# Kernel tuning notes

Hardware: AMD Instinct MI355X
Metric: run time of the kernel (lower is better)

The kernel has to match this reference:

```python
import jax, jax.numpy as jnp
import numpy as np

B, N, CH, DIM, SLOTS, ITERS, HID = 32, 4096, 256, 256, 11, 3, 512
EPS_ATTN = 1e-8
LN_EPS = 1e-3


def _ln(x, g, b):
    m = jnp.mean(x, axis=-1, keepdims=True)
    v = jnp.mean((x - m) ** 2, axis=-1, keepdims=True)
    return (x - m) * jax.lax.rsqrt(v + LN_EPS) * g + b


def setup_inputs() -> dict:
    key = jax.random.key(0)
    ks = jax.random.split(key, 16)
    s = lambda d: 1.0 / np.sqrt(d)
    return {
        "inputs": jax.random.normal(ks[0], (B, N, CH), jnp.float32),
        "noise": jax.random.normal(ks[1], (B, SLOTS, DIM), jnp.float32),
        "slots_mu": jax.random.uniform(ks[2], (1, 1, DIM), jnp.float32, -0.15, 0.15),
        "slots_log_sigma": jax.random.uniform(ks[3], (1, 1, DIM), jnp.float32, -0.15, 0.15),
        "Wq": jax.random.normal(ks[4], (DIM, DIM), jnp.float32) * s(DIM),
        "Wk": jax.random.normal(ks[5], (DIM, CH), jnp.float32) * s(CH),
        "Wv": jax.random.normal(ks[6], (DIM, CH), jnp.float32) * s(CH),
        "W_ih": jax.random.normal(ks[7], (3 * DIM, DIM), jnp.float32) * s(DIM),
        "W_hh": jax.random.normal(ks[8], (3 * DIM, DIM), jnp.float32) * s(DIM),
        "b_ih": jnp.zeros((3 * DIM,), jnp.float32),
        "b_hh": jnp.zeros((3 * DIM,), jnp.float32),
        "W1": jax.random.normal(ks[9], (HID, DIM), jnp.float32) * s(DIM),
        "b1": jnp.zeros((HID,), jnp.float32),
        "W2": jax.random.normal(ks[10], (DIM, HID), jnp.float32) * s(HID),
        "b2": jnp.zeros((DIM,), jnp.float32),
        "g_in": jnp.ones((CH,), jnp.float32), "be_in": jnp.zeros((CH,), jnp.float32),
        "g_sl": jnp.ones((DIM,), jnp.float32), "be_sl": jnp.zeros((DIM,), jnp.float32),
        "g_ff": jnp.ones((DIM,), jnp.float32), "be_ff": jnp.zeros((DIM,), jnp.float32),
    }


def reference(inputs, noise, slots_mu, slots_log_sigma, Wq, Wk, Wv, W_ih, W_hh,
              b_ih, b_hh, W1, b1, W2, b2, g_in, be_in, g_sl, be_sl, g_ff, be_ff):
    scale = DIM ** -0.5
    # reparameterized slot init: Normal(mu, exp(log_sigma))
    slots = slots_mu + jnp.exp(slots_log_sigma) * noise  # (B, S, D)
    x = _ln(inputs, g_in, be_in)
    k = jnp.einsum('bnc,dc->bnd', x, Wk)  # (B, N, D)
    v = jnp.einsum('bnc,dc->bnd', x, Wv)

    def gru(u, h):
        gi = u @ W_ih.T + b_ih
        gh = h @ W_hh.T + b_hh
        i_r, i_z, i_n = jnp.split(gi, 3, axis=-1)
        h_r, h_z, h_n = jnp.split(gh, 3, axis=-1)
        r = jax.nn.sigmoid(i_r + h_r)
        z = jax.nn.sigmoid(i_z + h_z)
        n = jnp.tanh(i_n + r * h_n)
        return (1.0 - z) * n + z * h

    for _ in range(ITERS):
        slots_prev = slots
        q = jnp.einsum('bid,ed->bie', _ln(slots, g_sl, be_sl), Wq)
        dots = jnp.einsum('bid,bjd->bij', q, k) * scale  # (B, S, N)
        attn = jax.nn.softmax(dots, axis=1) + EPS_ATTN   # competitive over slots
        attn = attn / jnp.sum(attn, axis=-1, keepdims=True)
        updates = jnp.einsum('bjd,bij->bid', v, attn)    # (B, S, D)
        slots = gru(updates.reshape(-1, DIM), slots_prev.reshape(-1, DIM)).reshape(B, -1, DIM)
        h = jax.nn.relu(_ln(slots, g_ff, be_ff) @ W1.T + b1)
        slots = slots + h @ W2.T + b2
    return slots
```

## Files before the change

### kernel.cpp

```cpp
#include <hip/hip_runtime.h>
#include <hip/hip_bf16.h>
#include <math.h>

typedef __bf16 bf16;
typedef __bf16 bf16x8 __attribute__((ext_vector_type(8)));
typedef float  f32x4  __attribute__((ext_vector_type(4)));

#define DEVI static __device__ __forceinline__

constexpr int B_ = 32, N_ = 4096, NS_ = 11, SP_ = 16, ITERS_ = 3;
constexpr int P_ = 32;
constexpr float LN_EPS_ = 1e-3f;
constexpr float EPS_ATTN_ = 1e-8f;

DEVI f32x4 mfma16(bf16x8 a, bf16x8 b, f32x4 c) {
  return __builtin_amdgcn_mfma_f32_16x16x32_bf16(a, b, c, 0, 0, 0);
}

DEVI float wsum64(float v) {
#pragma unroll
  for (int m = 32; m > 0; m >>= 1) v += __shfl_xor(v, m, 64);
  return v;
}

__global__ __launch_bounds__(256) void cast_weights(
    const float* __restrict__ Wq, const float* __restrict__ Wk,
    const float* __restrict__ Wv, const float* __restrict__ Wih,
    const float* __restrict__ Whh, const float* __restrict__ W1,
    const float* __restrict__ W2,
    bf16* __restrict__ cWkT, bf16* __restrict__ cWvT, bf16* __restrict__ cWq,
    bf16* __restrict__ cWih, bf16* __restrict__ cWhh, bf16* __restrict__ cW1,
    bf16* __restrict__ cW2) {
  const int idx = blockIdx.x * 256 + threadIdx.x;
  const int n0 = 256 * 256;
  const int n1 = n0 + 256 * 256;
  const int n2 = n1 + 256 * 256;
  const int n3 = n2 + 768 * 256;
  const int n4 = n3 + 768 * 256;
  const int n5 = n4 + 512 * 256;
  const int n6 = n5 + 256 * 512;
  if (idx < n0) {
    const int c = idx >> 8, d = idx & 255;
    cWkT[idx] = (bf16)Wk[d * 256 + c];
  } else if (idx < n1) {
    const int i = idx - n0; const int c = i >> 8, d = i & 255;
    cWvT[i] = (bf16)Wv[d * 256 + c];
  } else if (idx < n2) { const int i = idx - n1; cWq[i]  = (bf16)Wq[i];
  } else if (idx < n3) { const int i = idx - n2; cWih[i] = (bf16)Wih[i];
  } else if (idx < n4) { const int i = idx - n3; cWhh[i] = (bf16)Whh[i];
  } else if (idx < n5) { const int i = idx - n4; cW1[i]  = (bf16)W1[i];
  } else if (idx < n6) { const int i = idx - n5; cW2[i]  = (bf16)W2[i]; }
}

__global__ __launch_bounds__(256) void wfold_gemm(
    const bf16* __restrict__ Wih, const bf16* __restrict__ WvT,
    bf16* __restrict__ Wfold) {
  __shared__ bf16 At[32 * 256];
  const int mt = blockIdx.x, nt = blockIdx.y;
  const int tid = threadIdx.x, lane = tid & 63, wid = tid >> 6;
  const int l15 = lane & 15, gq = lane >> 4;
  const bf16* A = Wih + (size_t)mt * 32 * 256;
#pragma unroll
  for (int i = 0; i < 4; ++i) {
    const int idx = i * 256 + tid, row = idx >> 5, c = idx & 31;
    const bf16x8 v = *(const bf16x8*)(A + row * 256 + c * 8);
    const int byte = (row * 512 + c * 16) ^ ((row & 7) << 4);
    *(bf16x8*)((char*)At + byte) = v;
  }
  __syncthreads();
  const int wr = wid >> 1, wc = wid & 1;
  f32x4 acc[2] = {};
  for (int kk = 0; kk < 8; ++kk) {
    const int arow = wr * 16 + l15;
    const int byte = (arow * 512 + kk * 64 + gq * 16) ^ ((arow & 7) << 4);
    const bf16x8 af = *(const bf16x8*)((const char*)At + byte);
#pragma unroll
    for (int nn = 0; nn < 2; ++nn) {
      const bf16* wrow = WvT + (size_t)(nt * 64 + wc * 32 + nn * 16 + l15) * 256 + kk * 32 + gq * 8;
      acc[nn] = mfma16(af, *(const bf16x8*)wrow, acc[nn]);
    }
  }
#pragma unroll
  for (int nn = 0; nn < 2; ++nn)
#pragma unroll
    for (int r = 0; r < 4; ++r) {
      const int grow = mt * 32 + wr * 16 + gq * 4 + r;
      const int col = nt * 64 + wc * 32 + nn * 16 + l15;
      Wfold[(size_t)grow * 256 + col] = (bf16)acc[nn][r];
    }
}

__global__ __launch_bounds__(256) void init_slots(
    const float* __restrict__ mu, const float* __restrict__ lsig,
    const float* __restrict__ noise, float* __restrict__ slots,
    bf16* __restrict__ slots_bf) {
  const int idx = blockIdx.x * 256 + threadIdx.x;
  const int d = idx & 255;
  const float v = mu[d] + expf(lsig[d]) * noise[idx];
  slots[idx] = v;
  slots_bf[idx] = (bf16)v;
}

__global__ __launch_bounds__(256) void ln_castT(
    const float* __restrict__ inp, const float* __restrict__ g,
    const float* __restrict__ be, bf16* __restrict__ xhat,
    bf16* __restrict__ xhatT) {
  __shared__ bf16 At[128 * 256];
  const int mt = blockIdx.x;
  const int tid = threadIdx.x, lane = tid & 63, wid = tid >> 6;
  const int l15 = lane & 15, gq = lane >> 4;
  float4 gv[4], bv4[4];
#pragma unroll
  for (int u = 0; u < 4; ++u) {
    gv[u]  = ((const float4*)g)[l15 * 4 + u];
    bv4[u] = ((const float4*)be)[l15 * 4 + u];
  }
  for (int it8 = 0; it8 < 8; ++it8) {
    const int row = wid * 32 + it8 * 4 + gq;
    const size_t grow = (size_t)mt * 128 + row;
    const float4* rp = (const float4*)(inp + grow * 256 + l15 * 16);
    float4 x[4];
#pragma unroll
    for (int u = 0; u < 4; ++u) x[u] = rp[u];
    float s = 0.f, ss = 0.f;
#pragma unroll
    for (int u = 0; u < 4; ++u) {
      s += x[u].x + x[u].y + x[u].z + x[u].w;
      ss = fmaf(x[u].x, x[u].x, fmaf(x[u].y, x[u].y,
           fmaf(x[u].z, x[u].z, fmaf(x[u].w, x[u].w, ss))));
    }
#pragma unroll
    for (int m = 8; m > 0; m >>= 1) {
      s  += __shfl_xor(s,  m, 16);
      ss += __shfl_xor(ss, m, 16);
    }
    const float mean = s * (1.f / 256.f);
    const float rstd = rsqrtf(ss * (1.f / 256.f) - mean * mean + LN_EPS_);
    bf16x8 y0, y1;
#pragma unroll
    for (int u = 0; u < 2; ++u) {
      y0[u * 4 + 0] = (bf16)((x[u].x - mean) * rstd * gv[u].x + bv4[u].x);
      y0[u * 4 + 1] = (bf16)((x[u].y - mean) * rstd * gv[u].y + bv4[u].y);
      y0[u * 4 + 2] = (bf16)((x[u].z - mean) * rstd * gv[u].z + bv4[u].z);
      y0[u * 4 + 3] = (bf16)((x[u].w - mean) * rstd * gv[u].w + bv4[u].w);
      y1[u * 4 + 0] = (bf16)((x[2+u].x - mean) * rstd * gv[2+u].x + bv4[2+u].x);
      y1[u * 4 + 1] = (bf16)((x[2+u].y - mean) * rstd * gv[2+u].y + bv4[2+u].y);
      y1[u * 4 + 2] = (bf16)((x[2+u].z - mean) * rstd * gv[2+u].z + bv4[2+u].z);
      y1[u * 4 + 3] = (bf16)((x[2+u].w - mean) * rstd * gv[2+u].w + bv4[2+u].w);
    }
    bf16* orow = xhat + grow * 256 + l15 * 16;
    *(bf16x8*)orow       = y0;
    *(bf16x8*)(orow + 8) = y1;
    const int base = row * 512 + l15 * 32;
    const int sw = (row & 7) << 4;
    *(bf16x8*)((char*)At + ((base)      ^ sw)) = y0;
    *(bf16x8*)((char*)At + ((base + 16) ^ sw)) = y1;
  }
  __syncthreads();
  const int bidx = mt >> 5, jtile = (mt & 31) * 128;
#pragma unroll
  for (int i = 0; i < 16; ++i) {
    const int idx = i * 256 + tid;
    const int c = idx >> 4, j8 = (idx & 15) * 8;
    bf16x8 v;
#pragma unroll
    for (int e = 0; e < 8; ++e) {
      const int row = j8 + e;
      const int byte = (row * 512 + c * 2) ^ ((row & 7) << 4);
      v[e] = *(const bf16*)((const char*)At + byte);
    }
    *(bf16x8*)&xhatT[((size_t)(bidx * 256 + c)) * N_ + jtile + j8] = v;
  }
}

__global__ __launch_bounds__(256) void q_proj(
    const float* __restrict__ slots, const float* __restrict__ g,
    const float* __restrict__ be, const bf16* __restrict__ Wqb,
    const bf16* __restrict__ WkT, bf16* __restrict__ qpad) {
  const int i = blockIdx.x, b = blockIdx.y, t = threadIdx.x;
  bf16* out = qpad + (b * SP_ + i) * 256;
  if (i >= NS_) { out[t] = (bf16)0.f; return; }
  __shared__ float lnv[256], qd[256];
  __shared__ float red[8];
  const float x = slots[(b * NS_ + i) * 256 + t];
  float s = wsum64(x), ss = wsum64(x * x);
  const int lane = t & 63, w = t >> 6;
  if (lane == 0) { red[w] = s; red[4 + w] = ss; }
  __syncthreads();
  const float st = red[0] + red[1] + red[2] + red[3];
  const float qt = red[4] + red[5] + red[6] + red[7];
  const float mean = st / 256.f, var = qt / 256.f - mean * mean;
  const float rstd = rsqrtf(var + LN_EPS_);
  lnv[t] = (x - mean) * rstd * g[t] + be[t];
  __syncthreads();
  {
    float acc = 0.f;
    const bf16* wr = Wqb + (size_t)t * 256;
    for (int it = 0; it < 32; ++it) {
      const bf16x8 wv = *(const bf16x8*)(wr + it * 8);
      const float* u = &lnv[it * 8];
#pragma unroll
      for (int e = 0; e < 8; ++e) acc += (float)wv[e] * u[e];
    }
    qd[t] = acc;
  }
  __syncthreads();
  {
    float acc = 0.f;
    const bf16* wr = WkT + (size_t)t * 256;
    for (int it = 0; it < 32; ++it) {
      const bf16x8 wv = *(const bf16x8*)(wr + it * 8);
      const float* u = &qd[it * 8];
#pragma unroll
      for (int e = 0; e < 8; ++e) acc += (float)wv[e] * u[e];
    }
    out[t] = (bf16)(acc * 0.0625f);
  }
}

__global__ __launch_bounds__(256) void attn_part(
    const bf16* __restrict__ xhat, const bf16* __restrict__ xhatT,
    const bf16* __restrict__ qpad,
    float* __restrict__ num_part, float* __restrict__ den_part) {
  const int part = blockIdx.x, b = blockIdx.y;
  const int lane = threadIdx.x & 63, wid = threadIdx.x >> 6;
  const int l15 = lane & 15, gq = lane >> 4;
  const int jbase = part * 128 + wid * 32;
  const bf16* qrow = qpad + ((size_t)(b * SP_ + l15)) * 256;
  const bf16* kbase = xhat + ((size_t)(b * N_ + jbase)) * 256;
  const bf16* vtb = xhatT + ((size_t)b * 256) * N_ + jbase + gq * 8;
  __shared__ float nsw[2][4096];
  __shared__ float dens[4][16];

  bf16x8 bq[8];
#pragma unroll
  for (int kk = 0; kk < 8; ++kk)
    bq[kk] = *(const bf16x8*)(qrow + kk * 32 + gq * 8);
  bf16x8 v0[8];
#pragma unroll
  for (int dblk = 0; dblk < 8; ++dblk)
    v0[dblk] = *(const bf16x8*)(vtb + (size_t)(dblk * 16 + l15) * N_);

  float denacc = 0.f;
  float p0[4], p1[4];
#pragma unroll
  for (int T = 0; T < 2; ++T) {
    const bf16* krow = kbase + (size_t)(T * 16 + l15) * 256;
    f32x4 d = {0.f, 0.f, 0.f, 0.f};
#pragma unroll
    for (int kk = 0; kk < 8; ++kk) {
      const bf16x8 ak = *(const bf16x8*)(krow + kk * 32 + gq * 8);
      d = mfma16(ak, bq[kk], d);
    }
#pragma unroll
    for (int r = 0; r < 4; ++r) {
      float vmax = (l15 < NS_) ? d[r] : -1e30f;
#pragma unroll
      for (int mm = 8; mm > 0; mm >>= 1) vmax = fmaxf(vmax, __shfl_xor(vmax, mm, 16));
      const float e = (l15 < NS_) ? expf(d[r] - vmax) : 0.f;
      float ssum = e;
#pragma unroll
      for (int mm = 8; mm > 0; mm >>= 1) ssum += __shfl_xor(ssum, mm, 16);
      const float p = (l15 < NS_) ? (e / ssum + EPS_ATTN_) : 0.f;
      if (T == 0) p0[r] = p; else p1[r] = p;
      denacc += p;
    }
  }
  bf16x8 v1[8];
#pragma unroll
  for (int dblk = 0; dblk < 8; ++dblk)
    v1[dblk] = *(const bf16x8*)(vtb + (size_t)((8 + dblk) * 16 + l15) * N_);
  bf16x8 ap;
#pragma unroll
  for (int e = 0; e < 8; ++e) {
    const int srcl = l15 + ((2 * (gq & 1) + (e >> 2)) << 4);
    const float va = __shfl(p0[e & 3], srcl, 64);
    const float vb = __shfl(p1[e & 3], srcl, 64);
    ap[e] = (bf16)((gq < 2) ? va : vb);
  }
  f32x4 accN[16];
  __builtin_amdgcn_s_setprio(1);
#pragma unroll
  for (int dblk = 0; dblk < 8; ++dblk) {
    f32x4 z = {0.f, 0.f, 0.f, 0.f};
    accN[dblk] = mfma16(ap, v0[dblk], z);
  }
#pragma unroll
  for (int dblk = 0; dblk < 8; ++dblk) {
    f32x4 z = {0.f, 0.f, 0.f, 0.f};
    accN[8 + dblk] = mfma16(ap, v1[dblk], z);
  }
  __builtin_amdgcn_s_setprio(0);
  if (wid < 2) {
#pragma unroll
    for (int dblk = 0; dblk < 16; ++dblk)
#pragma unroll
      for (int r = 0; r < 4; ++r) {
        const int idx = (((4 * gq + r) * 256) + dblk * 16 + l15) ^ (gq << 4);
        nsw[wid][idx] = accN[dblk][r];
      }
  }
  __syncthreads();
  if (wid >= 2) {
#pragma unroll
    for (int dblk = 0; dblk < 16; ++dblk)
#pragma unroll
      for (int r = 0; r < 4; ++r) {
        const int idx = (((4 * gq + r) * 256) + dblk * 16 + l15) ^ (gq << 4);
        nsw[wid - 2][idx] += accN[dblk][r];
      }
  }
  float dtot = denacc + __shfl_xor(denacc, 16, 64);
  dtot += __shfl_xor(dtot, 32, 64);
  if (lane < 16) dens[wid][l15] = dtot;
  __syncthreads();
  const int t = threadIdx.x;
  if (t < NS_)
    den_part[(b * P_ + part) * NS_ + t] =
        dens[0][t] + dens[1][t] + dens[2][t] + dens[3][t];
  for (int r = 0; r < NS_; ++r) {
    const int swz = ((r >> 2) & 3) << 4;
    num_part[((size_t)((b * P_ + part) * NS_ + r)) * 256 + t] =
        nsw[0][(r * 256 + t) ^ swz] + nsw[1][(r * 256 + t) ^ swz];
  }
}

__global__ __launch_bounds__(256) void u0_reduce(
    const float* __restrict__ num_part, const float* __restrict__ den_part,
    bf16* __restrict__ u0b) {
  const int row = blockIdx.x, t = threadIdx.x;
  const int b = row / NS_, i = row % NS_;
  float nsum = 0.f;
  for (int p = 0; p < P_; ++p)
    nsum += num_part[((size_t)((b * P_ + p) * NS_ + i)) * 256 + t];
  float den = 0.f;
  for (int p = 0; p < P_; ++p) den += den_part[(b * P_ + p) * NS_ + i];
  u0b[(size_t)row * 256 + t] = (bf16)(nsum / den);
}

__global__ __launch_bounds__(256) void gates_gemm(
    const bf16* __restrict__ u0b, const bf16* __restrict__ hb,
    const bf16* __restrict__ Wfold, const bf16* __restrict__ Whh,
    float* __restrict__ gi, float* __restrict__ gh) {
  __shared__ bf16 At[32 * 256];
  const int mt = blockIdx.x, nt = blockIdx.y;
  const bool isI = nt < 12;
  const int ntile = isI ? nt : nt - 12;
  const bf16* A = (isI ? u0b : hb) + (size_t)mt * 32 * 256;
  const bf16* W = isI ? Wfold : Whh;
  float* out = isI ? gi : gh;
  const int tid = threadIdx.x, lane = tid & 63, wid = tid >> 6;
  const int l15 = lane & 15, gq = lane >> 4;
#pragma unroll
  for (int i = 0; i < 4; ++i) {
    const int idx = i * 256 + tid, row = idx >> 5, c = idx & 31;
    const bf16x8 v = *(const bf16x8*)(A + row * 256 + c * 8);
    const int byte = (row * 512 + c * 16) ^ ((row & 7) << 4);
    *(bf16x8*)((char*)At + byte) = v;
  }
  __syncthreads();
  const int wr = wid >> 1, wc = wid & 1;
  f32x4 acc[2] = {};
  for (int kk = 0; kk < 8; ++kk) {
    const int arow = wr * 16 + l15;
    const int byte = (arow * 512 + kk * 64 + gq * 16) ^ ((arow & 7) << 4);
    const bf16x8 af = *(const bf16x8*)((const char*)At + byte);
#pragma unroll
    for (int nn = 0; nn < 2; ++nn) {
      const bf16* wrow = W + (size_t)(ntile * 64 + wc * 32 + nn * 16 + l15) * 256 + kk * 32 + gq * 8;
      acc[nn] = mfma16(af, *(const bf16x8*)wrow, acc[nn]);
    }
  }
#pragma unroll
  for (int nn = 0; nn < 2; ++nn)
#pragma unroll
    for (int r = 0; r < 4; ++r) {
      const int grow = mt * 32 + wr * 16 + gq * 4 + r;
      const int col = ntile * 64 + wc * 32 + nn * 16 + l15;
      out[(size_t)grow * 768 + col] = acc[nn][r];
    }
}

__global__ __launch_bounds__(256) void gru_ew(
    const float* __restrict__ gi, const float* __restrict__ gh,
    const float* __restrict__ bih, const float* __restrict__ bhh,
    const float* __restrict__ slots_f, const float* __restrict__ gff,
    const float* __restrict__ beff, float* __restrict__ hn_out,
    bf16* __restrict__ ln_out) {
  const int row = blockIdx.x, t = threadIdx.x;
  __shared__ float red[8];
  const size_t g0 = (size_t)row * 768;
  const float ir = gi[g0 + t]       + bih[t];
  const float hr = gh[g0 + t]       + bhh[t];
  const float iz = gi[g0 + 256 + t] + bih[256 + t];
  const float hz = gh[g0 + 256 + t] + bhh[256 + t];
  const float inn = gi[g0 + 512 + t] + bih[512 + t];
  const float hnn = gh[g0 + 512 + t] + bhh[512 + t];
  const float h = slots_f[(size_t)row * 256 + t];
  const float r = 1.f / (1.f + expf(-(ir + hr)));
  const float z = 1.f / (1.f + expf(-(iz + hz)));
  const float n = tanhf(inn + r * hnn);
  const float hn = (1.f - z) * n + z * h;
  hn_out[(size_t)row * 256 + t] = hn;
  float s = wsum64(hn), ss = wsum64(hn * hn);
  const int lane = t & 63, w = t >> 6;
  if (lane == 0) { red[w] = s; red[4 + w] = ss; }
  __syncthreads();
  const float st = red[0] + red[1] + red[2] + red[3];
  const float qt = red[4] + red[5] + red[6] + red[7];
  const float mean = st / 256.f, var = qt / 256.f - mean * mean;
  const float rstd = rsqrtf(var + LN_EPS_);
  ln_out[(size_t)row * 256 + t] = (bf16)((hn - mean) * rstd * gff[t] + beff[t]);
}

__global__ __launch_bounds__(256) void w1_gemm(
    const bf16* __restrict__ lnb, const bf16* __restrict__ W1,
    const float* __restrict__ b1, bf16* __restrict__ h1b) {
  __shared__ bf16 At[32 * 256];
  const int mt = blockIdx.x, nt = blockIdx.y;
  const int tid = threadIdx.x, lane = tid & 63, wid = tid >> 6;
  const int l15 = lane & 15, gq = lane >> 4;
  const bf16* A = lnb + (size_t)mt * 32 * 256;
#pragma unroll
  for (int i = 0; i < 4; ++i) {
    const int idx = i * 256 + tid, row = idx >> 5, c = idx & 31;
    const bf16x8 v = *(const bf16x8*)(A + row * 256 + c * 8);
    const int byte = (row * 512 + c * 16) ^ ((row & 7) << 4);
    *(bf16x8*)((char*)At + byte) = v;
  }
  __syncthreads();
  const int wr = wid >> 1, wc = wid & 1;
  f32x4 acc[2] = {};
  for (int kk = 0; kk < 8; ++kk) {
    const int arow = wr * 16 + l15;
    const int byte = (arow * 512 + kk * 64 + gq * 16) ^ ((arow & 7) << 4);
    const bf16x8 af = *(const bf16x8*)((const char*)At + byte);
#pragma unroll
    for (int nn = 0; nn < 2; ++nn) {
      const bf16* wrow = W1 + (size_t)(nt * 64 + wc * 32 + nn * 16 + l15) * 256 + kk * 32 + gq * 8;
      acc[nn] = mfma16(af, *(const bf16x8*)wrow, acc[nn]);
    }
  }
#pragma unroll
  for (int nn = 0; nn < 2; ++nn)
#pragma unroll
    for (int r = 0; r < 4; ++r) {
      const int grow = mt * 32 + wr * 16 + gq * 4 + r;
      const int col = nt * 64 + wc * 32 + nn * 16 + l15;
      h1b[(size_t)grow * 512 + col] = (bf16)fmaxf(acc[nn][r] + b1[col], 0.f);
    }
}

__global__ __launch_bounds__(256) void w2_gemm(
    const bf16* __restrict__ h1b, const bf16* __restrict__ W2,
    const float* __restrict__ b2, const float* __restrict__ hn_in,
    float* __restrict__ sout, bf16* __restrict__ sbf) {
  __shared__ bf16 At[32 * 512];
  const int mt = blockIdx.x, nt = blockIdx.y;
  const int tid = threadIdx.x, lane = tid & 63, wid = tid >> 6;
  const int l15 = lane & 15, gq = lane >> 4;
  const bf16* A = h1b + (size_t)mt * 32 * 512;
#pragma unroll
  for (int i = 0; i < 8; ++i) {
    const int idx = i * 256 + tid, row = idx >> 6, c = idx & 63;
    const bf16x8 v = *(const bf16x8*)(A + row * 512 + c * 8);
    const int byte = (row * 1024 + c * 16) ^ ((row & 7) << 4);
    *(bf16x8*)((char*)At + byte) = v;
  }
  __syncthreads();
  const int wr = wid >> 1, wc = wid & 1;
  f32x4 acc[2] = {};
  for (int kk = 0; kk < 16; ++kk) {
    const int arow = wr * 16 + l15;
    const int byte = (arow * 1024 + kk * 64 + gq * 16) ^ ((arow & 7) << 4);
    const bf16x8 af = *(const bf16x8*)((const char*)At + byte);
#pragma unroll
    for (int nn = 0; nn < 2; ++nn) {
      const bf16* wrow = W2 + (size_t)(nt * 64 + wc * 32 + nn * 16 + l15) * 512 + kk * 32 + gq * 8;
      acc[nn] = mfma16(af, *(const bf16x8*)wrow, acc[nn]);
    }
  }
#pragma unroll
  for (int nn = 0; nn < 2; ++nn)
#pragma unroll
    for (int r = 0; r < 4; ++r) {
      const int grow = mt * 32 + wr * 16 + gq * 4 + r;
      const int col = nt * 64 + wc * 32 + nn * 16 + l15;
      const float v = hn_in[(size_t)grow * 256 + col] + acc[nn][r] + b2[col];
      sout[(size_t)grow * 256 + col] = v;
      sbf[(size_t)grow * 256 + col] = (bf16)v;
    }
}

extern "C" void kernel_launch(void* const* d_in, const int* in_sizes, int n_in,
                              void* d_out, int out_size, void* d_ws, size_t ws_size,
                              hipStream_t stream) {
  const float* inputs = (const float*)d_in[0];
  const float* noise  = (const float*)d_in[1];
  const float* mu     = (const float*)d_in[2];
  const float* lsig   = (const float*)d_in[3];
  const float* Wq     = (const float*)d_in[4];
  const float* Wk     = (const float*)d_in[5];
  const float* Wv     = (const float*)d_in[6];
  const float* Wih    = (const float*)d_in[7];
  const float* Whh    = (const float*)d_in[8];
  const float* bih    = (const float*)d_in[9];
  const float* bhh    = (const float*)d_in[10];
  const float* W1     = (const float*)d_in[11];
  const float* b1     = (const float*)d_in[12];
  const float* W2     = (const float*)d_in[13];
  const float* b2     = (const float*)d_in[14];
  const float* gin    = (const float*)d_in[15];
  const float* bein   = (const float*)d_in[16];
  const float* gsl    = (const float*)d_in[17];
  const float* besl   = (const float*)d_in[18];
  const float* gff    = (const float*)d_in[19];
  const float* beff   = (const float*)d_in[20];

  char* ws = (char*)d_ws;
  size_t off = 0;
  auto alloc = [&](size_t bytes) -> void* {
    void* p = ws + off;
    off += (bytes + 255) & ~(size_t)255;
    return p;
  };
  bf16*  xhat    = (bf16*) alloc((size_t)B_ * N_ * 256 * 2);
  bf16*  xhatT   = (bf16*) alloc((size_t)B_ * 256 * N_ * 2);
  bf16*  qpad    = (bf16*) alloc((size_t)B_ * SP_ * 256 * 2);
  bf16*  cWkT    = (bf16*) alloc(256 * 256 * 2);
  bf16*  cWvT    = (bf16*) alloc(256 * 256 * 2);
  bf16*  cWq     = (bf16*) alloc(256 * 256 * 2);
  bf16*  cWih    = (bf16*) alloc(768 * 256 * 2);
  bf16*  cWhh    = (bf16*) alloc(768 * 256 * 2);
  bf16*  cW1     = (bf16*) alloc(512 * 256 * 2);
  bf16*  cW2     = (bf16*) alloc(256 * 512 * 2);
  bf16*  Wfold   = (bf16*) alloc(768 * 256 * 2);
  float* slots   = (float*)alloc((size_t)352 * 256 * 4);
  bf16*  slots_bf= (bf16*) alloc((size_t)352 * 256 * 2);
  float* numpart = (float*)alloc((size_t)B_ * P_ * NS_ * 256 * 4);
  float* denpart = (float*)alloc((size_t)B_ * P_ * NS_ * 4);
  bf16*  u0b     = (bf16*) alloc((size_t)352 * 256 * 2);
  float* gi      = (float*)alloc((size_t)352 * 768 * 4);
  float* gh      = (float*)alloc((size_t)352 * 768 * 4);
  float* hn_f    = (float*)alloc((size_t)352 * 256 * 4);
  bf16*  ln_b    = (bf16*) alloc((size_t)352 * 256 * 2);
  bf16*  h1b     = (bf16*) alloc((size_t)352 * 512 * 2);
  (void)ws_size; (void)in_sizes; (void)n_in; (void)out_size;

  cast_weights<<<3328, 256, 0, stream>>>(Wq, Wk, Wv, Wih, Whh, W1, W2,
                                         cWkT, cWvT, cWq, cWih, cWhh, cW1, cW2);
  wfold_gemm<<<dim3(24, 4), 256, 0, stream>>>(cWih, cWvT, Wfold);
  init_slots<<<352, 256, 0, stream>>>(mu, lsig, noise, slots, slots_bf);
  ln_castT<<<1024, 256, 0, stream>>>(inputs, gin, bein, xhat, xhatT);
  for (int it = 0; it < ITERS_; ++it) {
    q_proj<<<dim3(SP_, B_), 256, 0, stream>>>(slots, gsl, besl, cWq, cWkT, qpad);
    attn_part<<<dim3(P_, B_), 256, 0, stream>>>(xhat, xhatT, qpad, numpart, denpart);
    u0_reduce<<<352, 256, 0, stream>>>(numpart, denpart, u0b);
    gates_gemm<<<dim3(11, 24), 256, 0, stream>>>(u0b, slots_bf, Wfold, cWhh, gi, gh);
    gru_ew<<<352, 256, 0, stream>>>(gi, gh, bih, bhh, slots, gff, beff, hn_f, ln_b);
    w1_gemm<<<dim3(11, 8), 256, 0, stream>>>(ln_b, cW1, b1, h1b);
    float* sout = (it == ITERS_ - 1) ? (float*)d_out : slots;
    w2_gemm<<<dim3(11, 4), 256, 0, stream>>>(h1b, cW2, b2, hn_f, sout, slots_bf);
  }
}
```

Baseline: 295.0 us.

## Drop transposed xhat copy; transpose V tiles through LDS inside attention kernel

The LayerNorm prologue no longer writes a transposed copy of the normalized inputs (a 64MB bf16 write). The attention kernel instead loads the row-major tile it already reads as K into per-wave swizzled LDS and gathers the transposed B-operand fragments from there, in two 128-column halves. Partial numerators are also stored in bf16 to halve the partial-reduction traffic, and ln_cast becomes a grid-stride kernel with 2048 blocks. The trade is extra LDS use and scalar LDS gathers in the hot loop, plus some precision loss on the summed partials.

```diff
diff --git a/kernel.cpp b/kernel.cpp
--- a/kernel.cpp
+++ b/kernel.cpp
@@ -3,6 +3,7 @@
 #include <math.h>
 
 typedef __bf16 bf16;
+typedef __bf16 bf16x4 __attribute__((ext_vector_type(4)));
 typedef __bf16 bf16x8 __attribute__((ext_vector_type(8)));
 typedef float  f32x4  __attribute__((ext_vector_type(4)));
 
@@ -101,12 +102,9 @@
   slots_bf[idx] = (bf16)v;
 }
 
-__global__ __launch_bounds__(256) void ln_castT(
+__global__ __launch_bounds__(256) void ln_cast(
     const float* __restrict__ inp, const float* __restrict__ g,
-    const float* __restrict__ be, bf16* __restrict__ xhat,
-    bf16* __restrict__ xhatT) {
-  __shared__ bf16 At[128 * 256];
-  const int mt = blockIdx.x;
+    const float* __restrict__ be, bf16* __restrict__ xhat) {
   const int tid = threadIdx.x, lane = tid & 63, wid = tid >> 6;
   const int l15 = lane & 15, gq = lane >> 4;
   float4 gv[4], bv4[4];
@@ -115,9 +113,10 @@
     gv[u]  = ((const float4*)g)[l15 * 4 + u];
     bv4[u] = ((const float4*)be)[l15 * 4 + u];
   }
-  for (int it8 = 0; it8 < 8; ++it8) {
-    const int row = wid * 32 + it8 * 4 + gq;
-    const size_t grow = (size_t)mt * 128 + row;
+  const int nwaves = gridDim.x * 4;
+  const int gw = blockIdx.x * 4 + wid;
+  for (int qi = gw; qi < (B_ * N_ / 4); qi += nwaves) {
+    const size_t grow = (size_t)qi * 4 + gq;
     const float4* rp = (const float4*)(inp + grow * 256 + l15 * 16);
     float4 x[4];
 #pragma unroll
@@ -151,25 +150,6 @@
     bf16* orow = xhat + grow * 256 + l15 * 16;
     *(bf16x8*)orow       = y0;
     *(bf16x8*)(orow + 8) = y1;
-    const int base = row * 512 + l15 * 32;
-    const int sw = (row & 7) << 4;
-    *(bf16x8*)((char*)At + ((base)      ^ sw)) = y0;
-    *(bf16x8*)((char*)At + ((base + 16) ^ sw)) = y1;
-  }
-  __syncthreads();
-  const int bidx = mt >> 5, jtile = (mt & 31) * 128;
-#pragma unroll
-  for (int i = 0; i < 16; ++i) {
-    const int idx = i * 256 + tid;
-    const int c = idx >> 4, j8 = (idx & 15) * 8;
-    bf16x8 v;
-#pragma unroll
-    for (int e = 0; e < 8; ++e) {
-      const int row = j8 + e;
-      const int byte = (row * 512 + c * 2) ^ ((row & 7) << 4);
-      v[e] = *(const bf16*)((const char*)At + byte);
-    }
-    *(bf16x8*)&xhatT[((size_t)(bidx * 256 + c)) * N_ + jtile + j8] = v;
   }
 }
 
@@ -219,27 +199,28 @@
 }
 
 __global__ __launch_bounds__(256) void attn_part(
-    const bf16* __restrict__ xhat, const bf16* __restrict__ xhatT,
-    const bf16* __restrict__ qpad,
-    float* __restrict__ num_part, float* __restrict__ den_part) {
+    const bf16* __restrict__ xhat, const bf16* __restrict__ qpad,
+    bf16* __restrict__ num_part, float* __restrict__ den_part) {
   const int part = blockIdx.x, b = blockIdx.y;
   const int lane = threadIdx.x & 63, wid = threadIdx.x >> 6;
   const int l15 = lane & 15, gq = lane >> 4;
   const int jbase = part * 128 + wid * 32;
   const bf16* qrow = qpad + ((size_t)(b * SP_ + l15)) * 256;
   const bf16* kbase = xhat + ((size_t)(b * N_ + jbase)) * 256;
-  const bf16* vtb = xhatT + ((size_t)b * 256) * N_ + jbase + gq * 8;
+  __shared__ bf16 vlds[4][4096];
   __shared__ float nsw[2][4096];
   __shared__ float dens[4][16];
-
+  char* myv = (char*)&vlds[wid][0];
+  const int srow = gq;
+
+  bf16x8 vst[8];
+#pragma unroll
+  for (int i = 0; i < 8; ++i)
+    vst[i] = *(const bf16x8*)(kbase + (size_t)(i * 4 + srow) * 256 + l15 * 8);
   bf16x8 bq[8];
 #pragma unroll
   for (int kk = 0; kk < 8; ++kk)
     bq[kk] = *(const bf16x8*)(qrow + kk * 32 + gq * 8);
-  bf16x8 v0[8];
-#pragma unroll
-  for (int dblk = 0; dblk < 8; ++dblk)
-    v0[dblk] = *(const bf16x8*)(vtb + (size_t)(dblk * 16 + l15) * N_);
 
   float denacc = 0.f;
   float p0[4], p1[4];
@@ -266,10 +247,6 @@
       denacc += p;
     }
   }
-  bf16x8 v1[8];
-#pragma unroll
-  for (int dblk = 0; dblk < 8; ++dblk)
-    v1[dblk] = *(const bf16x8*)(vtb + (size_t)((8 + dblk) * 16 + l15) * N_);
   bf16x8 ap;
 #pragma unroll
   for (int e = 0; e < 8; ++e) {
@@ -279,16 +256,47 @@
     ap[e] = (bf16)((gq < 2) ? va : vb);
   }
   f32x4 accN[16];
+#pragma unroll
+  for (int i = 0; i < 8; ++i) {
+    const int row = i * 4 + srow;
+    const int byte = (row * 256 + l15 * 16) ^ ((((row >> 3) & 3)) << 5);
+    *(bf16x8*)(myv + byte) = vst[i];
+  }
+#pragma unroll
+  for (int i = 0; i < 8; ++i)
+    vst[i] = *(const bf16x8*)(kbase + (size_t)(i * 4 + srow) * 256 + 128 + l15 * 8);
   __builtin_amdgcn_s_setprio(1);
 #pragma unroll
-  for (int dblk = 0; dblk < 8; ++dblk) {
+  for (int l = 0; l < 8; ++l) {
+    bf16x8 bvf;
+#pragma unroll
+    for (int e = 0; e < 8; ++e) {
+      const int row = 8 * gq + e;
+      const int byte = (row * 256 + l * 32 + l15 * 2) ^ ((((row >> 3) & 3)) << 5);
+      bvf[e] = *(const bf16*)(myv + byte);
+    }
     f32x4 z = {0.f, 0.f, 0.f, 0.f};
-    accN[dblk] = mfma16(ap, v0[dblk], z);
-  }
-#pragma unroll
-  for (int dblk = 0; dblk < 8; ++dblk) {
+    accN[l] = mfma16(ap, bvf, z);
+  }
+  __builtin_amdgcn_s_setprio(0);
+#pragma unroll
+  for (int i = 0; i < 8; ++i) {
+    const int row = i * 4 + srow;
+    const int byte = (row * 256 + l15 * 16) ^ ((((row >> 3) & 3)) << 5);
+    *(bf16x8*)(myv + byte) = vst[i];
+  }
+  __builtin_amdgcn_s_setprio(1);
+#pragma unroll
+  for (int l = 0; l < 8; ++l) {
+    bf16x8 bvf;
+#pragma unroll
+    for (int e = 0; e < 8; ++e) {
+      const int row = 8 * gq + e;
+      const int byte = (row * 256 + l * 32 + l15 * 2) ^ ((((row >> 3) & 3)) << 5);
+      bvf[e] = *(const bf16*)(myv + byte);
+    }
     f32x4 z = {0.f, 0.f, 0.f, 0.f};
-    accN[8 + dblk] = mfma16(ap, v1[dblk], z);
+    accN[8 + l] = mfma16(ap, bvf, z);
   }
   __builtin_amdgcn_s_setprio(0);
   if (wid < 2) {
@@ -321,18 +329,18 @@
   for (int r = 0; r < NS_; ++r) {
     const int swz = ((r >> 2) & 3) << 4;
     num_part[((size_t)((b * P_ + part) * NS_ + r)) * 256 + t] =
-        nsw[0][(r * 256 + t) ^ swz] + nsw[1][(r * 256 + t) ^ swz];
+        (bf16)(nsw[0][(r * 256 + t) ^ swz] + nsw[1][(r * 256 + t) ^ swz]);
   }
 }
 
 __global__ __launch_bounds__(256) void u0_reduce(
-    const float* __restrict__ num_part, const float* __restrict__ den_part,
+    const bf16* __restrict__ num_part, const float* __restrict__ den_part,
     bf16* __restrict__ u0b) {
   const int row = blockIdx.x, t = threadIdx.x;
   const int b = row / NS_, i = row % NS_;
   float nsum = 0.f;
   for (int p = 0; p < P_; ++p)
-    nsum += num_part[((size_t)((b * P_ + p) * NS_ + i)) * 256 + t];
+    nsum += (float)num_part[((size_t)((b * P_ + p) * NS_ + i)) * 256 + t];
   float den = 0.f;
   for (int p = 0; p < P_; ++p) den += den_part[(b * P_ + p) * NS_ + i];
   u0b[(size_t)row * 256 + t] = (bf16)(nsum / den);
@@ -525,7 +533,6 @@
     return p;
   };
   bf16*  xhat    = (bf16*) alloc((size_t)B_ * N_ * 256 * 2);
-  bf16*  xhatT   = (bf16*) alloc((size_t)B_ * 256 * N_ * 2);
   bf16*  qpad    = (bf16*) alloc((size_t)B_ * SP_ * 256 * 2);
   bf16*  cWkT    = (bf16*) alloc(256 * 256 * 2);
   bf16*  cWvT    = (bf16*) alloc(256 * 256 * 2);
@@ -537,7 +544,7 @@
   bf16*  Wfold   = (bf16*) alloc(768 * 256 * 2);
   float* slots   = (float*)alloc((size_t)352 * 256 * 4);
   bf16*  slots_bf= (bf16*) alloc((size_t)352 * 256 * 2);
-  float* numpart = (float*)alloc((size_t)B_ * P_ * NS_ * 256 * 4);
+  bf16*  numpart = (bf16*) alloc((size_t)B_ * P_ * NS_ * 256 * 2);
   float* denpart = (float*)alloc((size_t)B_ * P_ * NS_ * 4);
   bf16*  u0b     = (bf16*) alloc((size_t)352 * 256 * 2);
   float* gi      = (float*)alloc((size_t)352 * 768 * 4);
@@ -551,10 +558,10 @@
                                          cWkT, cWvT, cWq, cWih, cWhh, cW1, cW2);
   wfold_gemm<<<dim3(24, 4), 256, 0, stream>>>(cWih, cWvT, Wfold);
   init_slots<<<352, 256, 0, stream>>>(mu, lsig, noise, slots, slots_bf);
-  ln_castT<<<1024, 256, 0, stream>>>(inputs, gin, bein, xhat, xhatT);
+  ln_cast<<<2048, 256, 0, stream>>>(inputs, gin, bein, xhat);
   for (int it = 0; it < ITERS_; ++it) {
     q_proj<<<dim3(SP_, B_), 256, 0, stream>>>(slots, gsl, besl, cWq, cWkT, qpad);
-    attn_part<<<dim3(P_, B_), 256, 0, stream>>>(xhat, xhatT, qpad, numpart, denpart);
+    attn_part<<<dim3(P_, B_), 256, 0, stream>>>(xhat, qpad, numpart, denpart);
     u0_reduce<<<352, 256, 0, stream>>>(numpart, denpart, u0b);
     gates_gemm<<<dim3(11, 24), 256, 0, stream>>>(u0b, slots_bf, Wfold, cWhh, gi, gh);
     gru_ew<<<352, 256, 0, stream>>>(gi, gh, bih, bhh, slots, gff, beff, hn_f, ln_b);
```

Result: faster. 263.8 us (median of 2 runs) (-10.6%).
